# Performance work log

Measured on AMD Instinct MI355X. Metric: run time of the kernel, lower is better.

Reference implementation:

```python
import jax, jax.numpy as jnp
import numpy as np

RES = 512
N_LAYERS = 3
BATCH = 128
NUM_CLASSES = 10
LAMBDA = 5.32e-07
K = 2.0 * np.pi / LAMBDA  # module-level constant k in the original code
Z = 0.035                 # propagation distance d
DX = 1e-06                # pixel pitch


def _transfer_function(res):
    # Angular-spectrum Fresnel transfer function H(fx, fy), static numpy precompute.
    fx = np.fft.fftfreq(res, DX)
    FX, FY = np.meshgrid(fx, fx)
    H = np.exp(1j * K * Z) * np.exp(-1j * np.pi * LAMBDA * Z * (FX ** 2 + FY ** 2))
    return jnp.asarray(H.astype(np.complex64))


def setup_inputs() -> dict:
    key = jax.random.key(0)
    k1, k2, k3, k4 = jax.random.split(key, 4)
    x = jax.random.normal(k1, (BATCH, 1, RES, RES), dtype=jnp.float32)
    phases = jax.random.normal(k2, (N_LAYERS, RES, RES), dtype=jnp.float32) * 0.1
    fc_w = jax.random.normal(k3, (NUM_CLASSES, RES * RES), dtype=jnp.float32) * 0.01
    fc_b = jax.random.normal(k4, (NUM_CLASSES,), dtype=jnp.float32) * 0.01
    return {"x": x, "phases": phases, "fc_w": fc_w, "fc_b": fc_b}


def reference(x, phases, fc_w, fc_b):
    res = x.shape[-1]
    H = _transfer_function(res)  # (res, res) complex64
    field = x[:, 0].astype(jnp.complex64)  # (B, res, res)
    for i in range(phases.shape[0]):
        # phase-mask multiply, then Fresnel propagation: ifft2(fft2(field) * H)
        field = field * jnp.exp(1j * phases[i])
        field = jnp.fft.ifft2(jnp.fft.fft2(field, axes=(-2, -1)) * H, axes=(-2, -1))
    intensity = field.real ** 2 + field.imag ** 2  # |field|^2
    feat = intensity.reshape(x.shape[0], -1)
    return feat @ fc_w.T + fc_b
```

## Files before the change

### kernel.cpp

```cpp
#include <hip/hip_runtime.h>
#include <math.h>


#define PAD(i) ((i) + ((i) >> 4))
#define LSTR 545

typedef __attribute__((ext_vector_type(2))) _Float16 half2v;
typedef __attribute__((ext_vector_type(8))) _Float16 half8;

__device__ __forceinline__ void wave_lds_order() {
  asm volatile("" ::: "memory");
}

__device__ __forceinline__ float2 cadd(float2 a, float2 b){ return make_float2(a.x+b.x, a.y+b.y); }
__device__ __forceinline__ float2 csub(float2 a, float2 b){ return make_float2(a.x-b.x, a.y-b.y); }
__device__ __forceinline__ float2 cmul(float2 a, float2 b){ return make_float2(a.x*b.x - a.y*b.y, a.x*b.y + a.y*b.x); }

template<int S>
__device__ __forceinline__ float2 cmul_s(float2 a, float2 b) {
  return (S < 0) ? make_float2(a.x*b.x - a.y*b.y, a.x*b.y + a.y*b.x)
                 : make_float2(a.x*b.x + a.y*b.y, a.y*b.x - a.x*b.y);
}

template<int S>
__device__ __forceinline__ float2 crot(float2 z){
  return (S > 0) ? make_float2(-z.y, z.x) : make_float2(z.y, -z.x);
}

template<int S>
__device__ __forceinline__ void fft8(float2 v[8]) {
  const float sq = 0.70710678118654752440f;
  float2 t0 = cadd(v[0], v[4]), t1 = csub(v[0], v[4]);
  float2 t2 = cadd(v[2], v[6]), t3 = csub(v[2], v[6]);
  float2 E0 = cadd(t0, t2), E2 = csub(t0, t2);
  float2 rt3 = crot<S>(t3);
  float2 E1 = cadd(t1, rt3), E3 = csub(t1, rt3);
  float2 u0 = cadd(v[1], v[5]), u1 = csub(v[1], v[5]);
  float2 u2 = cadd(v[3], v[7]), u3 = csub(v[3], v[7]);
  float2 O0 = cadd(u0, u2), O2 = csub(u0, u2);
  float2 ru3 = crot<S>(u3);
  float2 O1 = cadd(u1, ru3), O3 = csub(u1, ru3);
  float2 O1w = make_float2(sq*(O1.x - (float)S*O1.y), sq*((float)S*O1.x + O1.y));
  float2 O2w = crot<S>(O2);
  float2 O3w = make_float2(-sq*(O3.x + (float)S*O3.y), sq*((float)S*O3.x - O3.y));
  v[0] = cadd(E0, O0);  v[4] = csub(E0, O0);
  v[1] = cadd(E1, O1w); v[5] = csub(E1, O1w);
  v[2] = cadd(E2, O2w); v[6] = csub(E2, O2w);
  v[3] = cadd(E3, O3w); v[7] = csub(E3, O3w);
}

__device__ __forceinline__ void mktw(float2 tw2[7], float2 tw3[7], int t) {
  float a2 = -6.28318530717958647692f * (float)(t & 7) / 64.0f;
  float a3 = -6.28318530717958647692f * (float)(t & 63) / 512.0f;
  float s2, c2; __sincosf(a2, &s2, &c2);
  float s3, c3; __sincosf(a3, &s3, &c3);
  float2 w2 = make_float2(c2, s2), w3 = make_float2(c3, s3);
  tw2[0] = w2; tw3[0] = w3;
  #pragma unroll
  for (int r = 1; r < 7; ++r) { tw2[r] = cmul(tw2[r-1], w2); tw3[r] = cmul(tw3[r-1], w3); }
}

template<int S>
__device__ __forceinline__ void fft512_w(float2 v[8], float2* __restrict__ B, int t,
                                         const float2 tw2[7], const float2 tw3[7]) {
  fft8<S>(v);
  #pragma unroll
  for (int r = 0; r < 8; ++r) B[PAD(8*t + r)] = v[r];
  wave_lds_order();
  #pragma unroll
  for (int r = 0; r < 8; ++r) v[r] = B[PAD(t + 64*r)];
  #pragma unroll
  for (int r = 1; r < 8; ++r) v[r] = cmul_s<S>(v[r], tw2[r-1]);
  fft8<S>(v);
  int d = ((t >> 3) << 6) | (t & 7);
  #pragma unroll
  for (int r = 0; r < 8; ++r) B[PAD(d + 8*r)] = v[r];
  wave_lds_order();
  #pragma unroll
  for (int r = 0; r < 8; ++r) v[r] = B[PAD(t + 64*r)];
  #pragma unroll
  for (int r = 1; r < 8; ++r) v[r] = cmul_s<S>(v[r], tw3[r-1]);
  fft8<S>(v);
}

__device__ __forceinline__ float2 h2f(half2v h) { return make_float2((float)h[0], (float)h[1]); }
__device__ __forceinline__ half2v f2h(float2 v) { half2v h; h[0] = (_Float16)v.x; h[1] = (_Float16)v.y; return h; }

__device__ __forceinline__ void store_T(float2* lds, const float2 v[8],
                                        int t, int w, int tid,
                                        half2v* __restrict__ dst, int rowbase) {
  __syncthreads();
  half2v* tile = (half2v*)lds;
  #pragma unroll
  for (int r = 0; r < 8; ++r) tile[w * 512 + t + 64*r] = f2h(v[r]);
  __syncthreads();
  int j = tid;
  half2v seg[8];
  #pragma unroll
  for (int w2 = 0; w2 < 8; ++w2) seg[w2] = tile[w2 * 512 + j];
  float4* d4 = (float4*)(dst + (size_t)j * 512 + rowbase);
  d4[0] = *(float4*)&seg[0];
  d4[1] = *(float4*)&seg[4];
  __syncthreads();
}


__global__ __launch_bounds__(256) void k_hinit(float2* __restrict__ hx,
                                               float2* __restrict__ hy) {
  int idx = blockIdx.x * 256 + threadIdx.x;
  int u = idx & 511;
  double f = (double)(u < 256 ? u : u - 512) * 1953.125;
  const double LAM = 5.32e-7, ZD = 0.035;
  const double PI = 3.14159265358979323846;
  double s, c;
  if (idx < 512) {
    double ang = -PI * LAM * ZD * f * f;
    sincos(ang, &s, &c);
    hx[u] = make_float2((float)c, (float)s);
  } else {
    double ang = (2.0 * PI / LAM) * ZD - PI * LAM * ZD * f * f;
    sincos(ang, &s, &c);
    const double sc = 1.0 / 512.0;
    hy[u] = make_float2((float)(c * sc), (float)(s * sc));
  }
}

__global__ __launch_bounds__(512) void k_r1(const float* __restrict__ x,
                                            const float* __restrict__ ph,
                                            half2v* __restrict__ Bout, int ng) {
  __shared__ float2 lds[8 * LSTR];
  int tid = threadIdx.x;
  int t = tid & 63, w = tid >> 6;
  float2 tw2[7], tw3[7];
  mktw(tw2, tw3, t);
  int grp = blockIdx.x;
  float pfx[8], pfp[8];
  if (grp < ng) {
    size_t row = (size_t)grp * 8 + w;
    const float* xr = x + row * 512;
    const float* pr = ph + (size_t)(row & 511) * 512;
    #pragma unroll
    for (int r = 0; r < 8; ++r) { pfx[r] = xr[t + 64*r]; pfp[r] = pr[t + 64*r]; }
  }
  while (grp < ng) {
    float2 v[8];
    #pragma unroll
    for (int r = 0; r < 8; ++r) {
      float sn, cs; __sincosf(pfp[r], &sn, &cs);
      v[r] = make_float2(pfx[r] * cs, pfx[r] * sn);
    }
    int next = grp + (int)gridDim.x;
    if (next < ng) {
      size_t nrow = (size_t)next * 8 + w;
      const float* xr = x + nrow * 512;
      const float* pr = ph + (size_t)(nrow & 511) * 512;
      #pragma unroll
      for (int r = 0; r < 8; ++r) { pfx[r] = xr[t + 64*r]; pfp[r] = pr[t + 64*r]; }
    }
    fft512_w<-1>(v, lds + w * LSTR, t, tw2, tw3);
    int bimg = (grp * 8) >> 9, rowbase = (grp * 8) & 511;
    store_T(lds, v, t, w, tid, Bout + (size_t)bimg * 262144, rowbase);
    grp = next;
  }
}

__global__ __launch_bounds__(512) void k_cmid(const half2v* __restrict__ Bin,
                                              half2v* __restrict__ Aout,
                                              const float2* __restrict__ hx,
                                              const float2* __restrict__ hy,
                                              int ng) {
  __shared__ float2 lds[8 * LSTR];
  int tid = threadIdx.x;
  int t = tid & 63, w = tid >> 6;
  float2 hyv[8];
  #pragma unroll
  for (int r = 0; r < 8; ++r) hyv[r] = hy[t + 64*r];
  float2 tw2[7], tw3[7];
  mktw(tw2, tw3, t);
  int grp = blockIdx.x;
  half2v pff[8];
  if (grp < ng) {
    int bimg = (grp * 8) >> 9, kx = (grp * 8 + w) & 511;
    const half2v* src = Bin + (size_t)bimg * 262144 + (size_t)kx * 512;
    #pragma unroll
    for (int r = 0; r < 8; ++r) pff[r] = src[t + 64*r];
  }
  while (grp < ng) {
    int bimg = (grp * 8) >> 9, kx = (grp * 8 + w) & 511;
    float2 v[8];
    #pragma unroll
    for (int r = 0; r < 8; ++r) v[r] = h2f(pff[r]);
    int next = grp + (int)gridDim.x;
    if (next < ng) {
      int nb = (next * 8) >> 9, nkx = (next * 8 + w) & 511;
      const half2v* src = Bin + (size_t)nb * 262144 + (size_t)nkx * 512;
      #pragma unroll
      for (int r = 0; r < 8; ++r) pff[r] = src[t + 64*r];
    }
    fft512_w<-1>(v, lds + w * LSTR, t, tw2, tw3);
    float2 hxv = hx[kx];
    #pragma unroll
    for (int r = 0; r < 8; ++r) v[r] = cmul(cmul(v[r], hyv[r]), hxv);
    fft512_w<1>(v, lds + w * LSTR, t, tw2, tw3);
    const float s512 = 1.0f / 512.0f;
    #pragma unroll
    for (int r = 0; r < 8; ++r) { v[r].x *= s512; v[r].y *= s512; }
    int rowbase = (grp * 8) & 511;
    store_T(lds, v, t, w, tid, Aout + (size_t)bimg * 262144, rowbase);
    grp = next;
  }
}

__global__ __launch_bounds__(512) void k_rmid(const half2v* __restrict__ Ain,
                                              half2v* __restrict__ Bout,
                                              const float* __restrict__ ph, int ng) {
  __shared__ float2 lds[8 * LSTR];
  int tid = threadIdx.x;
  int t = tid & 63, w = tid >> 6;
  float2 tw2[7], tw3[7];
  mktw(tw2, tw3, t);
  int grp = blockIdx.x;
  half2v pff[8]; float pfp[8];
  if (grp < ng) {
    int bimg = (grp * 8) >> 9, y = (grp * 8 + w) & 511;
    const half2v* src = Ain + (size_t)bimg * 262144 + (size_t)y * 512;
    const float* pr = ph + (size_t)y * 512;
    #pragma unroll
    for (int r = 0; r < 8; ++r) { pff[r] = src[t + 64*r]; pfp[r] = pr[t + 64*r]; }
  }
  while (grp < ng) {
    int bimg = (grp * 8) >> 9;
    float2 v[8]; float cur_p[8];
    #pragma unroll
    for (int r = 0; r < 8; ++r) { v[r] = h2f(pff[r]); cur_p[r] = pfp[r]; }
    int next = grp + (int)gridDim.x;
    if (next < ng) {
      int nb = (next * 8) >> 9, nyy = (next * 8 + w) & 511;
      const half2v* src = Ain + (size_t)nb * 262144 + (size_t)nyy * 512;
      const float* pr = ph + (size_t)nyy * 512;
      #pragma unroll
      for (int r = 0; r < 8; ++r) { pff[r] = src[t + 64*r]; pfp[r] = pr[t + 64*r]; }
    }
    fft512_w<1>(v, lds + w * LSTR, t, tw2, tw3);
    #pragma unroll
    for (int r = 0; r < 8; ++r) {
      float sn, cs; __sincosf(cur_p[r], &sn, &cs);
      v[r] = cmul(v[r], make_float2(cs, sn));
    }
    fft512_w<-1>(v, lds + w * LSTR, t, tw2, tw3);
    int rowbase = (grp * 8) & 511;
    store_T(lds, v, t, w, tid, Bout + (size_t)bimg * 262144, rowbase);
    grp = next;
  }
}

__global__ __launch_bounds__(256) void k_rlast(const half2v* __restrict__ F,
                                               const float* __restrict__ W,
                                               float* __restrict__ partial, int m) {
  __shared__ float2 lds[4 * LSTR];
  int tid = threadIdx.x;
  int t = tid & 63, rl = tid >> 6;
  int nq = (m + 3) >> 2;
  int y = blockIdx.x / nq;
  int q = blockIdx.x - y * nq;
  int g = q * 4 + rl;
  bool act = (g < m);
  const half2v* Fr = F + ((size_t)g * 262144 + (size_t)y * 512);
  float2 tw2[7], tw3[7];
  mktw(tw2, tw3, t);
  float2 v[8];
  #pragma unroll
  for (int r = 0; r < 8; ++r) {
    half2v h = act ? Fr[t + 64*r] : (half2v)(_Float16)0.0f;
    v[r] = h2f(h);
  }
  fft512_w<1>(v, lds + rl * LSTR, t, tw2, tw3);
  float acc[10];
  #pragma unroll
  for (int c = 0; c < 10; ++c) acc[c] = 0.0f;
  const float* Wy = W + (size_t)y * 512;
  #pragma unroll
  for (int r = 0; r < 8; ++r) {
    int e = t + 64*r;
    float I = v[r].x * v[r].x + v[r].y * v[r].y;
    #pragma unroll
    for (int c = 0; c < 10; ++c) acc[c] += I * Wy[(size_t)c * 262144 + e];
  }
  float mine = 0.0f;
  #pragma unroll
  for (int c = 0; c < 10; ++c) {
    float s = acc[c];
    #pragma unroll
    for (int off = 32; off > 0; off >>= 1) s += __shfl_xor(s, off, 64);
    if (t == c) mine = s;
  }
  if (act && t < 10)
    partial[((size_t)g * 10 + t) * 512 + y] = mine;
}

__global__ __launch_bounds__(64) void k_fc(const float* __restrict__ partial,
                                           const float* __restrict__ fc_b,
                                           float* __restrict__ out, int b0, int m) {
  int bid = blockIdx.x;
  int g = bid / 10, c = bid - g * 10;
  int t = threadIdx.x;
  const float* p = partial + ((size_t)g * 10 + c) * 512;
  float s = 0.0f;
  #pragma unroll
  for (int r = 0; r < 8; ++r) s += p[t + 64*r];
  #pragma unroll
  for (int off = 32; off > 0; off >>= 1) s += __shfl_xor(s, off, 64);
  if (t == 0) out[(size_t)(b0 + g) * 10 + c] = s + fc_b[c];
}


extern "C" void kernel_launch(void* const* d_in, const int* in_sizes, int n_in,
                              void* d_out, int out_size, void* d_ws, size_t ws_size,
                              hipStream_t stream) {
  const float* x    = (const float*)d_in[0];
  const float* ph   = (const float*)d_in[1];
  const float* fc_w = (const float*)d_in[2];
  const float* fc_b = (const float*)d_in[3];
  float* out = (float*)d_out;

  const size_t IMG = 262144;
  const size_t PER_IMG = 2 * IMG * sizeof(half2v) + 512 * 10 * sizeof(float);
  float2* hx = (float2*)d_ws;
  float2* hy = hx + 512;
  size_t hdr = 1024 * sizeof(float2);
  size_t avail = (ws_size > hdr) ? ws_size - hdr : 0;
  int M = (int)(avail / PER_IMG);
  if (M < 1) M = 1;
  if (M > 128) M = 128;
  half2v* A = (half2v*)((char*)d_ws + hdr);
  half2v* B = A + (size_t)M * IMG;
  float* part = (float*)(B + (size_t)M * IMG);

  hipLaunchKernelGGL(k_hinit, dim3(4), dim3(256), 0, stream, hx, hy);

  for (int b0 = 0; b0 < 128; b0 += M) {
    int m = (128 - b0 < M) ? (128 - b0) : M;
    int ng = m * 64;
    int g512 = ng < 1024 ? ng : 1024;
    int nq = (m + 3) >> 2;
    hipLaunchKernelGGL(k_r1,   dim3(g512), dim3(512), 0, stream,
                       x + (size_t)b0 * IMG, ph, B, ng);
    hipLaunchKernelGGL(k_cmid, dim3(g512), dim3(512), 0, stream,
                       (const half2v*)B, A, (const float2*)hx, (const float2*)hy, ng);
    hipLaunchKernelGGL(k_rmid, dim3(g512), dim3(512), 0, stream,
                       (const half2v*)A, B, ph + IMG, ng);
    hipLaunchKernelGGL(k_cmid, dim3(g512), dim3(512), 0, stream,
                       (const half2v*)B, A, (const float2*)hx, (const float2*)hy, ng);
    hipLaunchKernelGGL(k_rmid, dim3(g512), dim3(512), 0, stream,
                       (const half2v*)A, B, ph + 2 * IMG, ng);
    hipLaunchKernelGGL(k_cmid, dim3(g512), dim3(512), 0, stream,
                       (const half2v*)B, A, (const float2*)hx, (const float2*)hy, ng);
    hipLaunchKernelGGL(k_rlast, dim3(512 * nq), dim3(256), 0, stream,
                       (const half2v*)A, fc_w, part, m);
    hipLaunchKernelGGL(k_fc,   dim3(m * 10), dim3(64), 0, stream, part, fc_b, out, b0, m);
  }
}
```

Before: 796.8 us.

## Process 16 rows per block so transposed stores write 64-byte segments

```diff
diff --git a/kernel.cpp b/kernel.cpp
--- a/kernel.cpp
+++ b/kernel.cpp
@@ -86,21 +86,28 @@
 __device__ __forceinline__ float2 h2f(half2v h) { return make_float2((float)h[0], (float)h[1]); }
 __device__ __forceinline__ half2v f2h(float2 v) { half2v h; h[0] = (_Float16)v.x; h[1] = (_Float16)v.y; return h; }
 
-__device__ __forceinline__ void store_T(float2* lds, const float2 v[8],
-                                        int t, int w, int tid,
-                                        half2v* __restrict__ dst, int rowbase) {
+__device__ __forceinline__ void store_T16(float2* lds, const float2 v[8],
+                                          int t, int w, int tid,
+                                          half2v* __restrict__ dst, int rowbase) {
   __syncthreads();
   half2v* tile = (half2v*)lds;
   #pragma unroll
   for (int r = 0; r < 8; ++r) tile[w * 512 + t + 64*r] = f2h(v[r]);
   __syncthreads();
-  int j = tid;
-  half2v seg[8];
-  #pragma unroll
-  for (int w2 = 0; w2 < 8; ++w2) seg[w2] = tile[w2 * 512 + j];
-  float4* d4 = (float4*)(dst + (size_t)j * 512 + rowbase);
-  d4[0] = *(float4*)&seg[0];
-  d4[1] = *(float4*)&seg[4];
+  if (tid < 512) {
+    int j = tid;
+    half8 o[4];
+    #pragma unroll
+    for (int b = 0; b < 4; ++b) {
+      #pragma unroll
+      for (int k = 0; k < 4; ++k) {
+        half2v e = tile[(4*b + k) * 512 + j];
+        o[b][2*k] = e[0]; o[b][2*k + 1] = e[1];
+      }
+    }
+    half8* d8 = (half8*)(dst + (size_t)j * 512 + rowbase);
+    d8[0] = o[0]; d8[1] = o[1]; d8[2] = o[2]; d8[3] = o[3];
+  }
   __syncthreads();
 }
 
@@ -125,10 +132,10 @@
   }
 }
 
-__global__ __launch_bounds__(512) void k_r1(const float* __restrict__ x,
-                                            const float* __restrict__ ph,
-                                            half2v* __restrict__ Bout, int ng) {
-  __shared__ float2 lds[8 * LSTR];
+__global__ __launch_bounds__(1024) void k_r1(const float* __restrict__ x,
+                                             const float* __restrict__ ph,
+                                             half2v* __restrict__ Bout, int ng) {
+  __shared__ float2 lds[16 * LSTR];
   int tid = threadIdx.x;
   int t = tid & 63, w = tid >> 6;
   float2 tw2[7], tw3[7];
@@ -136,8 +143,8 @@
   int grp = blockIdx.x;
   float pfx[8], pfp[8];
   if (grp < ng) {
-    size_t row = (size_t)grp * 8 + w;
-    const float* xr = x + row * 512;
+    int row = grp * 16 + w;
+    const float* xr = x + (size_t)row * 512;
     const float* pr = ph + (size_t)(row & 511) * 512;
     #pragma unroll
     for (int r = 0; r < 8; ++r) { pfx[r] = xr[t + 64*r]; pfp[r] = pr[t + 64*r]; }
@@ -151,70 +158,73 @@
     }
     int next = grp + (int)gridDim.x;
     if (next < ng) {
-      size_t nrow = (size_t)next * 8 + w;
-      const float* xr = x + nrow * 512;
+      int nrow = next * 16 + w;
+      const float* xr = x + (size_t)nrow * 512;
       const float* pr = ph + (size_t)(nrow & 511) * 512;
       #pragma unroll
       for (int r = 0; r < 8; ++r) { pfx[r] = xr[t + 64*r]; pfp[r] = pr[t + 64*r]; }
     }
     fft512_w<-1>(v, lds + w * LSTR, t, tw2, tw3);
-    int bimg = (grp * 8) >> 9, rowbase = (grp * 8) & 511;
-    store_T(lds, v, t, w, tid, Bout + (size_t)bimg * 262144, rowbase);
+    int bimg = grp >> 5, rowbase = (grp * 16) & 511;
+    store_T16(lds, v, t, w, tid, Bout + (size_t)bimg * 262144, rowbase);
     grp = next;
   }
 }
 
-__global__ __launch_bounds__(512) void k_cmid(const half2v* __restrict__ Bin,
-                                              half2v* __restrict__ Aout,
-                                              const float2* __restrict__ hx,
-                                              const float2* __restrict__ hy,
-                                              int ng) {
-  __shared__ float2 lds[8 * LSTR];
+__global__ __launch_bounds__(1024) void k_cmid(const half2v* __restrict__ Bin,
+                                               half2v* __restrict__ Aout,
+                                               const float2* __restrict__ hx,
+                                               const float2* __restrict__ hy,
+                                               int ng) {
+  __shared__ float2 lds[16 * LSTR];
+  __shared__ float2 hyl[512];
   int tid = threadIdx.x;
   int t = tid & 63, w = tid >> 6;
-  float2 hyv[8];
-  #pragma unroll
-  for (int r = 0; r < 8; ++r) hyv[r] = hy[t + 64*r];
+  if (tid < 512) hyl[tid] = hy[tid];
   float2 tw2[7], tw3[7];
   mktw(tw2, tw3, t);
   int grp = blockIdx.x;
   half2v pff[8];
   if (grp < ng) {
-    int bimg = (grp * 8) >> 9, kx = (grp * 8 + w) & 511;
-    const half2v* src = Bin + (size_t)bimg * 262144 + (size_t)kx * 512;
+    int row = grp * 16 + w;
+    const half2v* src = Bin + (size_t)(row >> 9) * 262144
+                            + (size_t)(row & 511) * 512;
     #pragma unroll
     for (int r = 0; r < 8; ++r) pff[r] = src[t + 64*r];
   }
+  __syncthreads();
   while (grp < ng) {
-    int bimg = (grp * 8) >> 9, kx = (grp * 8 + w) & 511;
+    int row = grp * 16 + w;
+    int kx = row & 511;
     float2 v[8];
     #pragma unroll
     for (int r = 0; r < 8; ++r) v[r] = h2f(pff[r]);
     int next = grp + (int)gridDim.x;
     if (next < ng) {
-      int nb = (next * 8) >> 9, nkx = (next * 8 + w) & 511;
-      const half2v* src = Bin + (size_t)nb * 262144 + (size_t)nkx * 512;
+      int nrow = next * 16 + w;
+      const half2v* src = Bin + (size_t)(nrow >> 9) * 262144
+                              + (size_t)(nrow & 511) * 512;
       #pragma unroll
       for (int r = 0; r < 8; ++r) pff[r] = src[t + 64*r];
     }
     fft512_w<-1>(v, lds + w * LSTR, t, tw2, tw3);
     float2 hxv = hx[kx];
     #pragma unroll
-    for (int r = 0; r < 8; ++r) v[r] = cmul(cmul(v[r], hyv[r]), hxv);
+    for (int r = 0; r < 8; ++r) v[r] = cmul(cmul(v[r], hyl[t + 64*r]), hxv);
     fft512_w<1>(v, lds + w * LSTR, t, tw2, tw3);
     const float s512 = 1.0f / 512.0f;
     #pragma unroll
     for (int r = 0; r < 8; ++r) { v[r].x *= s512; v[r].y *= s512; }
-    int rowbase = (grp * 8) & 511;
-    store_T(lds, v, t, w, tid, Aout + (size_t)bimg * 262144, rowbase);
+    int bimg = grp >> 5, rowbase = (grp * 16) & 511;
+    store_T16(lds, v, t, w, tid, Aout + (size_t)bimg * 262144, rowbase);
     grp = next;
   }
 }
 
-__global__ __launch_bounds__(512) void k_rmid(const half2v* __restrict__ Ain,
-                                              half2v* __restrict__ Bout,
-                                              const float* __restrict__ ph, int ng) {
-  __shared__ float2 lds[8 * LSTR];
+__global__ __launch_bounds__(1024) void k_rmid(const half2v* __restrict__ Ain,
+                                               half2v* __restrict__ Bout,
+                                               const float* __restrict__ ph, int ng) {
+  __shared__ float2 lds[16 * LSTR];
   int tid = threadIdx.x;
   int t = tid & 63, w = tid >> 6;
   float2 tw2[7], tw3[7];
@@ -222,34 +232,40 @@
   int grp = blockIdx.x;
   half2v pff[8]; float pfp[8];
   if (grp < ng) {
-    int bimg = (grp * 8) >> 9, y = (grp * 8 + w) & 511;
-    const half2v* src = Ain + (size_t)bimg * 262144 + (size_t)y * 512;
-    const float* pr = ph + (size_t)y * 512;
+    int row = grp * 16 + w;
+    const half2v* src = Ain + (size_t)(row >> 9) * 262144
+                            + (size_t)(row & 511) * 512;
+    const float* pr = ph + (size_t)(row & 511) * 512;
     #pragma unroll
     for (int r = 0; r < 8; ++r) { pff[r] = src[t + 64*r]; pfp[r] = pr[t + 64*r]; }
   }
   while (grp < ng) {
-    int bimg = (grp * 8) >> 9;
-    float2 v[8]; float cur_p[8];
-    #pragma unroll
-    for (int r = 0; r < 8; ++r) { v[r] = h2f(pff[r]); cur_p[r] = pfp[r]; }
+    float2 v[8];
+    #pragma unroll
+    for (int r = 0; r < 8; ++r) v[r] = h2f(pff[r]);
     int next = grp + (int)gridDim.x;
     if (next < ng) {
-      int nb = (next * 8) >> 9, nyy = (next * 8 + w) & 511;
-      const half2v* src = Ain + (size_t)nb * 262144 + (size_t)nyy * 512;
-      const float* pr = ph + (size_t)nyy * 512;
-      #pragma unroll
-      for (int r = 0; r < 8; ++r) { pff[r] = src[t + 64*r]; pfp[r] = pr[t + 64*r]; }
+      int nrow = next * 16 + w;
+      const half2v* src = Ain + (size_t)(nrow >> 9) * 262144
+                              + (size_t)(nrow & 511) * 512;
+      #pragma unroll
+      for (int r = 0; r < 8; ++r) pff[r] = src[t + 64*r];
     }
     fft512_w<1>(v, lds + w * LSTR, t, tw2, tw3);
     #pragma unroll
     for (int r = 0; r < 8; ++r) {
-      float sn, cs; __sincosf(cur_p[r], &sn, &cs);
+      float sn, cs; __sincosf(pfp[r], &sn, &cs);
       v[r] = cmul(v[r], make_float2(cs, sn));
     }
+    if (next < ng) {
+      int nrow = next * 16 + w;
+      const float* pr = ph + (size_t)(nrow & 511) * 512;
+      #pragma unroll
+      for (int r = 0; r < 8; ++r) pfp[r] = pr[t + 64*r];
+    }
     fft512_w<-1>(v, lds + w * LSTR, t, tw2, tw3);
-    int rowbase = (grp * 8) & 511;
-    store_T(lds, v, t, w, tid, Bout + (size_t)bimg * 262144, rowbase);
+    int bimg = grp >> 5, rowbase = (grp * 16) & 511;
+    store_T16(lds, v, t, w, tid, Bout + (size_t)bimg * 262144, rowbase);
     grp = next;
   }
 }
@@ -340,20 +356,20 @@
 
   for (int b0 = 0; b0 < 128; b0 += M) {
     int m = (128 - b0 < M) ? (128 - b0) : M;
-    int ng = m * 64;
-    int g512 = ng < 1024 ? ng : 1024;
+    int ng = m * 32;
+    int g1024 = ng < 512 ? ng : 512;
     int nq = (m + 3) >> 2;
-    hipLaunchKernelGGL(k_r1,   dim3(g512), dim3(512), 0, stream,
+    hipLaunchKernelGGL(k_r1,   dim3(g1024), dim3(1024), 0, stream,
                        x + (size_t)b0 * IMG, ph, B, ng);
-    hipLaunchKernelGGL(k_cmid, dim3(g512), dim3(512), 0, stream,
+    hipLaunchKernelGGL(k_cmid, dim3(g1024), dim3(1024), 0, stream,
                        (const half2v*)B, A, (const float2*)hx, (const float2*)hy, ng);
-    hipLaunchKernelGGL(k_rmid, dim3(g512), dim3(512), 0, stream,
+    hipLaunchKernelGGL(k_rmid, dim3(g1024), dim3(1024), 0, stream,
                        (const half2v*)A, B, ph + IMG, ng);
-    hipLaunchKernelGGL(k_cmid, dim3(g512), dim3(512), 0, stream,
+    hipLaunchKernelGGL(k_cmid, dim3(g1024), dim3(1024), 0, stream,
                        (const half2v*)B, A, (const float2*)hx, (const float2*)hy, ng);
-    hipLaunchKernelGGL(k_rmid, dim3(g512), dim3(512), 0, stream,
+    hipLaunchKernelGGL(k_rmid, dim3(g1024), dim3(1024), 0, stream,
                        (const half2v*)A, B, ph + 2 * IMG, ng);
-    hipLaunchKernelGGL(k_cmid, dim3(g512), dim3(512), 0, stream,
+    hipLaunchKernelGGL(k_cmid, dim3(g1024), dim3(1024), 0, stream,
                        (const half2v*)B, A, (const float2*)hx, (const float2*)hy, ng);
     hipLaunchKernelGGL(k_rlast, dim3(512 * nq), dim3(256), 0, stream,
                        (const half2v*)A, fc_w, part, m);
```

Result: slower. 840.2 us (+5.4%).
